# Optimization experiments

Measured on AMD Instinct MI355X. Metric: run time of the kernel, lower is better.

Reference implementation:

```python
import jax, jax.numpy as jnp
import numpy as np

HEAD_SIZE = 64
INPUT_SIZE = 1024
B, T = 8, 2048


def setup_inputs() -> dict:
    key = jax.random.key(0)
    kx, kq, kk, kv = jax.random.split(key, 4)
    x = jax.random.normal(kx, (B, T, INPUT_SIZE), dtype=jnp.float32)
    s = 1.0 / np.sqrt(INPUT_SIZE)
    Wq = jax.random.uniform(kq, (INPUT_SIZE, HEAD_SIZE), minval=-s, maxval=s, dtype=jnp.float32)
    Wk = jax.random.uniform(kk, (INPUT_SIZE, HEAD_SIZE), minval=-s, maxval=s, dtype=jnp.float32)
    Wv = jax.random.uniform(kv, (INPUT_SIZE, HEAD_SIZE), minval=-s, maxval=s, dtype=jnp.float32)
    return {"x": x, "Wq": Wq, "Wk": Wk, "Wv": Wv}


def reference(x, Wq, Wk, Wv):
    # Faithful to the torch module: scores = K @ Q^T (note: keys times queries^T),
    # causal mask on upper triangle of that matrix, softmax over last axis,
    # dropout treated as identity (eval), then scores @ V.
    q = jnp.einsum('bti,ih->bth', x, Wq)  # [B,T,H]
    k = jnp.einsum('bti,ih->bth', x, Wk)
    v = jnp.einsum('bti,ih->bth', x, Wv)
    scale = HEAD_SIZE ** -0.5
    scores = jnp.einsum('bth,bsh->bts', k, q) * scale  # [B,T,T] = K Q^T
    Tlen = x.shape[1]
    causal = jnp.tril(jnp.ones((Tlen, Tlen), dtype=bool))
    scores = jnp.where(causal, scores, -jnp.inf)
    w = jax.nn.softmax(scores, axis=-1)
    out = jnp.einsum('bts,bsh->bth', w, v)  # [B,T,H]
    return out
```

## Files before the change

kernel.cpp:

```cpp
#include <hip/hip_runtime.h>

typedef __bf16 bf16_t;
typedef bf16_t bf16x8 __attribute__((ext_vector_type(8)));
typedef float f32x4 __attribute__((ext_vector_type(4)));

#define NB 8
#define TT 2048
#define DIN 1024
#define HH 64
#define MM (NB * TT)

__device__ __forceinline__ unsigned short f2bf(float f) {
    unsigned int u = __float_as_uint(f);
    u += 0x7fffu + ((u >> 16) & 1u);
    return (unsigned short)(u >> 16);
}

__device__ __forceinline__ int block_detect_f32(const unsigned int* __restrict__ xw,
                                                int tid, int* sflag) {
    if (tid < 64) {
        unsigned int u = xw[tid];
        unsigned int e = (u >> 7) & 0xFFu;
        unsigned long long m = __ballot(e >= 100u && e <= 150u);
        if (tid == 0) *sflag = (__popcll(m) < 48) ? 1 : 0;
    }
    __syncthreads();
    return *sflag;
}

__global__ __launch_bounds__(256) void transpose_w_kernel(
    const void* __restrict__ Wq, const void* __restrict__ Wk,
    const void* __restrict__ Wv, const unsigned int* __restrict__ xw,
    unsigned short* __restrict__ Wt) {
    __shared__ int sflag;
    __shared__ unsigned short ts[64][68];
    const int tid = threadIdx.x;
    const int isf32 = block_detect_f32(xw, tid, &sflag);
    const int w = blockIdx.x >> 4, kt = blockIdx.x & 15;
    const void* W = (w == 0) ? Wq : (w == 1) ? Wk : Wv;
    const int kk = tid >> 4, nn = (tid & 15) * 4;
#pragma unroll
    for (int j = 0; j < 4; ++j) {
        int k = kk + j * 16;
        if (isf32) {
            float4 f = *(const float4*)((const float*)W + (size_t)(kt * 64 + k) * 64 + nn);
            ts[k][nn + 0] = f2bf(f.x); ts[k][nn + 1] = f2bf(f.y);
            ts[k][nn + 2] = f2bf(f.z); ts[k][nn + 3] = f2bf(f.w);
        } else {
            *(uint2*)&ts[k][nn] =
                *(const uint2*)((const unsigned short*)W + (size_t)(kt * 64 + k) * 64 + nn);
        }
    }
    __syncthreads();
    const int n = tid >> 2, k0 = (tid & 3) * 16;
    unsigned short tmp[16];
#pragma unroll
    for (int j = 0; j < 16; ++j) tmp[j] = ts[k0 + j][n];
    unsigned short* dst = Wt + (size_t)(w * 64 + n) * 1024 + kt * 64 + k0;
    *(uint4*)(dst + 0) = *(uint4*)&tmp[0];
    *(uint4*)(dst + 8) = *(uint4*)&tmp[8];
}

__global__ __launch_bounds__(256) void proj_kernel(
    const void* __restrict__ xraw, const unsigned short* __restrict__ Wt,
    unsigned short* __restrict__ qbuf, unsigned short* __restrict__ kbuf,
    unsigned short* __restrict__ vtbuf) {
    __shared__ int sflag;
    __shared__ __align__(16) unsigned short xs[64][72];
    __shared__ __align__(16) unsigned short wts[192][72];

    const int tid = threadIdx.x;
    const int isf32 = block_detect_f32((const unsigned int*)xraw, tid, &sflag);
    const int m0 = blockIdx.x * 64;
    const int wave = tid >> 6, lane = tid & 63, quad = lane >> 4, l15 = lane & 15;
    const int rw = wave & 1, cw = wave >> 1;

    f32x4 acc[2][6];
#pragma unroll
    for (int rt = 0; rt < 2; ++rt)
#pragma unroll
        for (int ct = 0; ct < 6; ++ct)
            acc[rt][ct] = (f32x4){0.f, 0.f, 0.f, 0.f};

    const float* xf = (const float*)xraw;
    const unsigned short* xb = (const unsigned short*)xraw;

    const int xrow = tid >> 2, xkb = (tid & 3) * 16;

    float4 px[4];
    uint4  pxb[2];
    uint4  pw[6];

    auto prefetch = [&](int k0) {
        if (isf32) {
            const float* gp = xf + (size_t)(m0 + xrow) * DIN + k0 + xkb;
#pragma unroll
            for (int j = 0; j < 4; ++j) px[j] = *(const float4*)(gp + j * 4);
        } else {
            const unsigned short* gp = xb + (size_t)(m0 + xrow) * DIN + k0 + xkb;
            pxb[0] = *(const uint4*)(gp + 0);
            pxb[1] = *(const uint4*)(gp + 8);
        }
#pragma unroll
        for (int j = 0; j < 6; ++j) {
            int c = tid + j * 256;
            int row = c >> 3, kc = c & 7;
            pw[j] = *(const uint4*)(Wt + (size_t)row * 1024 + k0 + kc * 8);
        }
    };

    prefetch(0);

    for (int it = 0; it < 16; ++it) {
        __syncthreads();
        if (isf32) {
            unsigned short t[16];
#pragma unroll
            for (int j = 0; j < 4; ++j) {
                t[j * 4 + 0] = f2bf(px[j].x); t[j * 4 + 1] = f2bf(px[j].y);
                t[j * 4 + 2] = f2bf(px[j].z); t[j * 4 + 3] = f2bf(px[j].w);
            }
            *(uint4*)&xs[xrow][xkb + 0] = *(uint4*)&t[0];
            *(uint4*)&xs[xrow][xkb + 8] = *(uint4*)&t[8];
        } else {
            *(uint4*)&xs[xrow][xkb + 0] = pxb[0];
            *(uint4*)&xs[xrow][xkb + 8] = pxb[1];
        }
#pragma unroll
        for (int j = 0; j < 6; ++j) {
            int c = tid + j * 256;
            int row = c >> 3, kc = c & 7;
            *(uint4*)&wts[row][kc * 8] = pw[j];
        }
        __syncthreads();

        if (it < 15) prefetch((it + 1) * 64);

#pragma unroll
        for (int ks = 0; ks < 2; ++ks) {
            bf16x8 a[2], b[6];
#pragma unroll
            for (int rt = 0; rt < 2; ++rt)
                a[rt] = *(const bf16x8*)&xs[rw * 32 + rt * 16 + l15][ks * 32 + quad * 8];
#pragma unroll
            for (int ct = 0; ct < 6; ++ct)
                b[ct] = *(const bf16x8*)&wts[cw * 96 + ct * 16 + l15][ks * 32 + quad * 8];
#pragma unroll
            for (int rt = 0; rt < 2; ++rt)
#pragma unroll
                for (int ct = 0; ct < 6; ++ct)
                    acc[rt][ct] = __builtin_amdgcn_mfma_f32_16x16x32_bf16(
                        a[rt], b[ct], acc[rt][ct], 0, 0, 0);
        }
    }

#pragma unroll
    for (int rt = 0; rt < 2; ++rt)
#pragma unroll
        for (int ct = 0; ct < 6; ++ct) {
            int n = cw * 96 + ct * 16 + l15;
            int wsel = n >> 6, nn = n & 63;
#pragma unroll
            for (int reg = 0; reg < 4; ++reg) {
                int m = m0 + rw * 32 + rt * 16 + quad * 4 + reg;
                unsigned short bv = f2bf(acc[rt][ct][reg]);
                if (wsel == 0)      qbuf[(size_t)m * HH + nn] = bv;
                else if (wsel == 1) kbuf[(size_t)m * HH + nn] = bv;
                else {
                    int bb = m >> 11, t = m & 2047;
                    vtbuf[((size_t)bb * HH + nn) * TT + t] = bv;
                }
            }
        }
}

__global__ __launch_bounds__(256) void attn_kernel(
    const unsigned short* __restrict__ rowbuf,
    const unsigned short* __restrict__ colbuf,
    const unsigned short* __restrict__ vtbuf,
    float* __restrict__ O_part,
    float* __restrict__ l_part) {

    __shared__ __align__(16) unsigned short Qr_s[64][72];
    __shared__ __align__(16) unsigned short Kc_s[64][72];
    __shared__ __align__(16) unsigned short Vt_s[64][72];
    __shared__ __align__(16) unsigned short P_s[4][16][72];

    const int tid  = threadIdx.x;
    const int bx   = blockIdx.x;
    const int b    = blockIdx.y;
    int rt, ch;
    if (bx < 8)       { rt = bx;                 ch = 0; }
    else if (bx < 24) { rt = 8 + ((bx - 8) >> 1);  ch = (bx - 8) & 1; }
    else if (bx < 48) { rt = 16 + (bx - 24) / 3;   ch = (bx - 24) % 3; }
    else              { rt = 24 + ((bx - 48) >> 2); ch = (bx - 48) & 3; }
    const int nct = min(8, rt + 1 - ch * 8);
    const int t0 = rt * 64;
    const int slot = b * 80 + bx;

    const int wave = tid >> 6, lane = tid & 63, quad = lane >> 4, l15 = lane & 15;
    const int sr = tid >> 2, sc = (tid & 3) * 16;

    {
        const uint4* g = (const uint4*)(rowbuf + ((size_t)b * TT + t0 + sr) * HH + sc);
        *(uint4*)&Qr_s[sr][sc + 0] = g[0];
        *(uint4*)&Qr_s[sr][sc + 8] = g[1];
    }

    f32x4 o[4];
#pragma unroll
    for (int c = 0; c < 4; ++c) o[c] = (f32x4){0.f, 0.f, 0.f, 0.f};
    float ls[4] = {0.f, 0.f, 0.f, 0.f};

    const float SCL2 = 0.125f * 1.4426950408889634f;

    for (int i = 0; i < nct; ++i) {
        const int stc = ch * 8 + i;
        const int s0 = stc * 64;
        {
            const uint4* gk = (const uint4*)(colbuf + ((size_t)b * TT + s0 + sr) * HH + sc);
            uint4 k0 = gk[0], k1 = gk[1];
            const uint4* gv = (const uint4*)(vtbuf + ((size_t)b * HH + sr) * TT + s0 + sc);
            uint4 v0 = gv[0], v1 = gv[1];
            *(uint4*)&Kc_s[sr][sc + 0] = k0;
            *(uint4*)&Kc_s[sr][sc + 8] = k1;
            *(uint4*)&Vt_s[sr][sc + 0] = v0;
            *(uint4*)&Vt_s[sr][sc + 8] = v1;
        }
        __syncthreads();

        f32x4 scf[4];
#pragma unroll
        for (int c = 0; c < 4; ++c) scf[c] = (f32x4){0.f, 0.f, 0.f, 0.f};
#pragma unroll
        for (int ks = 0; ks < 2; ++ks) {
            bf16x8 a = *(const bf16x8*)&Qr_s[wave * 16 + l15][ks * 32 + quad * 8];
#pragma unroll
            for (int c = 0; c < 4; ++c) {
                bf16x8 bb = *(const bf16x8*)&Kc_s[c * 16 + l15][ks * 32 + quad * 8];
                scf[c] = __builtin_amdgcn_mfma_f32_16x16x32_bf16(a, bb, scf[c], 0, 0, 0);
            }
        }

        const bool diag = (stc == rt);
#pragma unroll
        for (int r = 0; r < 4; ++r) {
            const int tg = t0 + wave * 16 + quad * 4 + r;
#pragma unroll
            for (int c = 0; c < 4; ++c) {
                float arg = fmaf(scf[c][r], SCL2, -30.f);
                if (diag && (s0 + c * 16 + l15) > tg) arg = -200.f;
                float p = __builtin_amdgcn_exp2f(arg);
                P_s[wave][quad * 4 + r][c * 16 + l15] = f2bf(p);
                ls[r] += p;
            }
        }
#pragma unroll
        for (int ks = 0; ks < 2; ++ks) {
            bf16x8 ap = *(const bf16x8*)&P_s[wave][l15][ks * 32 + quad * 8];
#pragma unroll
            for (int c = 0; c < 4; ++c) {
                bf16x8 bv = *(const bf16x8*)&Vt_s[c * 16 + l15][ks * 32 + quad * 8];
                o[c] = __builtin_amdgcn_mfma_f32_16x16x32_bf16(ap, bv, o[c], 0, 0, 0);
            }
        }
        __syncthreads();
    }

#pragma unroll
    for (int r = 0; r < 4; ++r) {
#pragma unroll
        for (int off = 1; off < 16; off <<= 1) ls[r] += __shfl_xor(ls[r], off);
    }
    if (l15 == 0) {
#pragma unroll
        for (int r = 0; r < 4; ++r)
            l_part[(size_t)slot * 64 + wave * 16 + quad * 4 + r] = ls[r];
    }
#pragma unroll
    for (int c = 0; c < 4; ++c)
#pragma unroll
        for (int r = 0; r < 4; ++r)
            O_part[(size_t)slot * 4096 + (wave * 16 + quad * 4 + r) * 64 + c * 16 + l15] = o[c][r];
}

__global__ __launch_bounds__(256) void combine_kernel(
    const float* __restrict__ O_part, const float* __restrict__ l_part,
    const unsigned int* __restrict__ xw, void* __restrict__ outraw) {
    __shared__ int sflag;
    const int tid = threadIdx.x;
    const int isf32 = block_detect_f32(xw, tid, &sflag);
    const int rt = blockIdx.x, b = blockIdx.y;
    const int nch = rt / 8 + 1;
    const int off = (rt < 8) ? rt : (rt < 16) ? 8 + 2 * (rt - 8)
                   : (rt < 24) ? 24 + 3 * (rt - 16) : 48 + 4 * (rt - 24);
    const int slot0 = b * 80 + off;

    const int row = tid >> 2, cb = (tid & 3) * 16;
    f32x4 a[4];
#pragma unroll
    for (int q = 0; q < 4; ++q) a[q] = (f32x4){0.f, 0.f, 0.f, 0.f};
    float l = 0.f;
    for (int j = 0; j < nch; ++j) {
        const f32x4* p = (const f32x4*)(O_part + (size_t)(slot0 + j) * 4096 + row * 64 + cb);
#pragma unroll
        for (int q = 0; q < 4; ++q) a[q] += p[q];
        l += l_part[(size_t)(slot0 + j) * 64 + row];
    }
    const float inv = 1.f / l;
    const size_t base = ((size_t)b * TT + rt * 64 + row) * HH + cb;
    if (isf32) {
        float* outf = (float*)outraw;
#pragma unroll
        for (int q = 0; q < 4; ++q) {
            f32x4 v = a[q] * inv;
            *(f32x4*)(outf + base + q * 4) = v;
        }
    } else {
        unsigned short h[16];
#pragma unroll
        for (int q = 0; q < 4; ++q)
#pragma unroll
            for (int e = 0; e < 4; ++e) h[q * 4 + e] = f2bf(a[q][e] * inv);
        unsigned short* outb = (unsigned short*)outraw;
        *(uint4*)(outb + base + 0) = *(uint4*)&h[0];
        *(uint4*)(outb + base + 8) = *(uint4*)&h[8];
    }
}

extern "C" void kernel_launch(void* const* d_in, const int* in_sizes, int n_in,
                              void* d_out, int out_size, void* d_ws, size_t ws_size,
                              hipStream_t stream) {
    const void* x  = d_in[0];
    const void* Wq = d_in[1];
    const void* Wk = d_in[2];
    const void* Wv = d_in[3];
    unsigned short* ws = (unsigned short*)d_ws;

    unsigned short* qbuf  = ws;
    unsigned short* kbuf  = ws + (size_t)MM * HH;
    unsigned short* vtbuf = ws + (size_t)2 * MM * HH;
    unsigned short* wtbuf = ws + (size_t)3 * MM * HH;
    float* O_part = (float*)(ws + (size_t)3 * MM * HH + 3 * 65536);
    float* l_part = O_part + (size_t)640 * 4096;

    hipLaunchKernelGGL(transpose_w_kernel, dim3(48), dim3(256), 0, stream,
                       Wq, Wk, Wv, (const unsigned int*)x, wtbuf);
    hipLaunchKernelGGL(proj_kernel, dim3(256), dim3(256), 0, stream,
                       x, wtbuf, qbuf, kbuf, vtbuf);
    hipLaunchKernelGGL(attn_kernel, dim3(80, 8), dim3(256), 0, stream,
                       kbuf, qbuf, vtbuf, O_part, l_part);
    hipLaunchKernelGGL(combine_kernel, dim3(32, 8), dim3(256), 0, stream,
                       O_part, l_part, (const unsigned int*)x, d_out);
}
```

Baseline: 159.6 us.

## Split projection over N, async-load weights to LDS, fuse combine into attention

The projection kernel now splits the 192 output columns across two grid rows (512 blocks instead of 256) and loads the weight tile directly into LDS with global_load_lds, which frees registers and allows two blocks per CU. The separate combine kernel is removed. The last attention block to finish each row tile, detected with an atomic counter that the transpose kernel zeroes, now does the normalisation and writes the output. This removes one launch and adds more parallelism in the projection, at the cost of reading x twice and adding fence and atomic overhead.

New measurement: 278.9 us. +74.8%, slower.

```diff
diff --git a/kernel.cpp b/kernel.cpp
--- a/kernel.cpp
+++ b/kernel.cpp
@@ -14,6 +14,12 @@
     unsigned int u = __float_as_uint(f);
     u += 0x7fffu + ((u >> 16) & 1u);
     return (unsigned short)(u >> 16);
+}
+
+__device__ __forceinline__ void async16(void* l, const void* g) {
+    __builtin_amdgcn_global_load_lds(
+        (const __attribute__((address_space(1))) unsigned int*)g,
+        (__attribute__((address_space(3))) unsigned int*)l, 16, 0, 0);
 }
 
 __device__ __forceinline__ int block_detect_f32(const unsigned int* __restrict__ xw,
@@ -31,10 +37,11 @@
 __global__ __launch_bounds__(256) void transpose_w_kernel(
     const void* __restrict__ Wq, const void* __restrict__ Wk,
     const void* __restrict__ Wv, const unsigned int* __restrict__ xw,
-    unsigned short* __restrict__ Wt) {
+    unsigned short* __restrict__ Wt, int* __restrict__ ctr) {
     __shared__ int sflag;
     __shared__ unsigned short ts[64][68];
     const int tid = threadIdx.x;
+    if (blockIdx.x == 0) ctr[tid] = 0;
     const int isf32 = block_detect_f32(xw, tid, &sflag);
     const int w = blockIdx.x >> 4, kt = blockIdx.x & 15;
     const void* W = (w == 0) ? Wq : (w == 1) ? Wk : Wv;
@@ -61,56 +68,67 @@
     *(uint4*)(dst + 8) = *(uint4*)&tmp[8];
 }
 
-__global__ __launch_bounds__(256) void proj_kernel(
+#define XR 72
+#define WROWC 9
+
+__global__ __launch_bounds__(256, 2) void proj_kernel(
     const void* __restrict__ xraw, const unsigned short* __restrict__ Wt,
     unsigned short* __restrict__ qbuf, unsigned short* __restrict__ kbuf,
     unsigned short* __restrict__ vtbuf) {
     __shared__ int sflag;
-    __shared__ __align__(16) unsigned short xs[64][72];
-    __shared__ __align__(16) unsigned short wts[192][72];
+    __shared__ __align__(16) unsigned short xs[64 * XR];
+    __shared__ __align__(16) unsigned char wlds[96 * WROWC * 16];
 
     const int tid = threadIdx.x;
     const int isf32 = block_detect_f32((const unsigned int*)xraw, tid, &sflag);
     const int m0 = blockIdx.x * 64;
+    const int nh = blockIdx.y;
     const int wave = tid >> 6, lane = tid & 63, quad = lane >> 4, l15 = lane & 15;
     const int rw = wave & 1, cw = wave >> 1;
 
-    f32x4 acc[2][6];
-#pragma unroll
-    for (int rt = 0; rt < 2; ++rt)
-#pragma unroll
-        for (int ct = 0; ct < 6; ++ct)
-            acc[rt][ct] = (f32x4){0.f, 0.f, 0.f, 0.f};
-
     const float* xf = (const float*)xraw;
     const unsigned short* xb = (const unsigned short*)xraw;
-
-    const int xrow = tid >> 2, xkb = (tid & 3) * 16;
-
+    const unsigned char* wg = (const unsigned char*)Wt;
+
+    const unsigned char* wsrc[4];
+    unsigned int wdst[4];
+    int nw = 0;
+#pragma unroll
+    for (int j = 0; j < 4; ++j) {
+        int c = (wave + 4 * j) * 64 + lane;
+        if (c < 864) {
+            int R = c / WROWC, cc = c % WROWC;
+            int ccu = (cc > 7) ? 0 : cc;
+            wsrc[nw] = wg + (size_t)(nh * 96 + R) * 2048 + ccu * 16;
+            wdst[nw] = c * 16;
+            ++nw;
+        }
+    }
+
+    const int xr = tid >> 2, xc = (tid & 3) * 16;
     float4 px[4];
     uint4  pxb[2];
-    uint4  pw[6];
-
-    auto prefetch = [&](int k0) {
+    auto ldx = [&](int k0) {
         if (isf32) {
-            const float* gp = xf + (size_t)(m0 + xrow) * DIN + k0 + xkb;
-#pragma unroll
-            for (int j = 0; j < 4; ++j) px[j] = *(const float4*)(gp + j * 4);
+            const float* g = xf + (size_t)(m0 + xr) * DIN + k0 + xc;
+#pragma unroll
+            for (int j = 0; j < 4; ++j) px[j] = *(const float4*)(g + j * 4);
         } else {
-            const unsigned short* gp = xb + (size_t)(m0 + xrow) * DIN + k0 + xkb;
-            pxb[0] = *(const uint4*)(gp + 0);
-            pxb[1] = *(const uint4*)(gp + 8);
-        }
-#pragma unroll
-        for (int j = 0; j < 6; ++j) {
-            int c = tid + j * 256;
-            int row = c >> 3, kc = c & 7;
-            pw[j] = *(const uint4*)(Wt + (size_t)row * 1024 + k0 + kc * 8);
+            const unsigned short* g = xb + (size_t)(m0 + xr) * DIN + k0 + xc;
+            pxb[0] = *(const uint4*)(g + 0);
+            pxb[1] = *(const uint4*)(g + 8);
         }
     };
 
-    prefetch(0);
-
+    f32x4 acc[2][3];
+#pragma unroll
+    for (int rt = 0; rt < 2; ++rt)
+#pragma unroll
+        for (int ct = 0; ct < 3; ++ct)
+            acc[rt][ct] = (f32x4){0.f, 0.f, 0.f, 0.f};
+
+    ldx(0);
+    size_t woff = 0;
     for (int it = 0; it < 16; ++it) {
         __syncthreads();
         if (isf32) {
@@ -120,35 +138,33 @@
                 t[j * 4 + 0] = f2bf(px[j].x); t[j * 4 + 1] = f2bf(px[j].y);
                 t[j * 4 + 2] = f2bf(px[j].z); t[j * 4 + 3] = f2bf(px[j].w);
             }
-            *(uint4*)&xs[xrow][xkb + 0] = *(uint4*)&t[0];
-            *(uint4*)&xs[xrow][xkb + 8] = *(uint4*)&t[8];
+            *(uint4*)&xs[xr * XR + xc + 0] = *(uint4*)&t[0];
+            *(uint4*)&xs[xr * XR + xc + 8] = *(uint4*)&t[8];
         } else {
-            *(uint4*)&xs[xrow][xkb + 0] = pxb[0];
-            *(uint4*)&xs[xrow][xkb + 8] = pxb[1];
-        }
-#pragma unroll
-        for (int j = 0; j < 6; ++j) {
-            int c = tid + j * 256;
-            int row = c >> 3, kc = c & 7;
-            *(uint4*)&wts[row][kc * 8] = pw[j];
-        }
+            *(uint4*)&xs[xr * XR + xc + 0] = pxb[0];
+            *(uint4*)&xs[xr * XR + xc + 8] = pxb[1];
+        }
+        for (int j = 0; j < nw; ++j) async16(&wlds[wdst[j]], wsrc[j] + woff);
+        woff += 128;
         __syncthreads();
 
-        if (it < 15) prefetch((it + 1) * 64);
+        if (it < 15) ldx((it + 1) * 64);
 
 #pragma unroll
         for (int ks = 0; ks < 2; ++ks) {
-            bf16x8 a[2], b[6];
+            bf16x8 a[2], b[3];
 #pragma unroll
             for (int rt = 0; rt < 2; ++rt)
-                a[rt] = *(const bf16x8*)&xs[rw * 32 + rt * 16 + l15][ks * 32 + quad * 8];
-#pragma unroll
-            for (int ct = 0; ct < 6; ++ct)
-                b[ct] = *(const bf16x8*)&wts[cw * 96 + ct * 16 + l15][ks * 32 + quad * 8];
+                a[rt] = *(const bf16x8*)
+                    &xs[(rw * 32 + rt * 16 + l15) * XR + ks * 32 + quad * 8];
+#pragma unroll
+            for (int ct = 0; ct < 3; ++ct)
+                b[ct] = *(const bf16x8*)
+                    &wlds[(cw * 48 + ct * 16 + l15) * (WROWC * 16) + ks * 64 + quad * 16];
 #pragma unroll
             for (int rt = 0; rt < 2; ++rt)
 #pragma unroll
-                for (int ct = 0; ct < 6; ++ct)
+                for (int ct = 0; ct < 3; ++ct)
                     acc[rt][ct] = __builtin_amdgcn_mfma_f32_16x16x32_bf16(
                         a[rt], b[ct], acc[rt][ct], 0, 0, 0);
         }
@@ -157,8 +173,8 @@
 #pragma unroll
     for (int rt = 0; rt < 2; ++rt)
 #pragma unroll
-        for (int ct = 0; ct < 6; ++ct) {
-            int n = cw * 96 + ct * 16 + l15;
+        for (int ct = 0; ct < 3; ++ct) {
+            int n = nh * 96 + cw * 48 + ct * 16 + l15;
             int wsel = n >> 6, nn = n & 63;
 #pragma unroll
             for (int reg = 0; reg < 4; ++reg) {
@@ -179,14 +195,20 @@
     const unsigned short* __restrict__ colbuf,
     const unsigned short* __restrict__ vtbuf,
     float* __restrict__ O_part,
-    float* __restrict__ l_part) {
-
+    float* __restrict__ l_part,
+    int* __restrict__ ctr,
+    const unsigned int* __restrict__ xw,
+    void* __restrict__ outraw) {
+
+    __shared__ int sflag;
     __shared__ __align__(16) unsigned short Qr_s[64][72];
     __shared__ __align__(16) unsigned short Kc_s[64][72];
     __shared__ __align__(16) unsigned short Vt_s[64][72];
     __shared__ __align__(16) unsigned short P_s[4][16][72];
+    __shared__ int slast;
 
     const int tid  = threadIdx.x;
+    const int isf32 = block_detect_f32(xw, tid, &sflag);
     const int bx   = blockIdx.x;
     const int b    = blockIdx.y;
     int rt, ch;
@@ -282,20 +304,21 @@
 #pragma unroll
         for (int r = 0; r < 4; ++r)
             O_part[(size_t)slot * 4096 + (wave * 16 + quad * 4 + r) * 64 + c * 16 + l15] = o[c][r];
-}
-
-__global__ __launch_bounds__(256) void combine_kernel(
-    const float* __restrict__ O_part, const float* __restrict__ l_part,
-    const unsigned int* __restrict__ xw, void* __restrict__ outraw) {
-    __shared__ int sflag;
-    const int tid = threadIdx.x;
-    const int isf32 = block_detect_f32(xw, tid, &sflag);
-    const int rt = blockIdx.x, b = blockIdx.y;
+
     const int nch = rt / 8 + 1;
+    __threadfence();
+    __syncthreads();
+    if (tid == 0) {
+        int prev = atomicAdd(&ctr[b * 32 + rt], 1);
+        slast = (prev == nch - 1) ? 1 : 0;
+    }
+    __syncthreads();
+    if (!slast) return;
+    __threadfence();
+
     const int off = (rt < 8) ? rt : (rt < 16) ? 8 + 2 * (rt - 8)
                    : (rt < 24) ? 24 + 3 * (rt - 16) : 48 + 4 * (rt - 24);
     const int slot0 = b * 80 + off;
-
     const int row = tid >> 2, cb = (tid & 3) * 16;
     f32x4 a[4];
 #pragma unroll
@@ -343,13 +366,13 @@
     unsigned short* wtbuf = ws + (size_t)3 * MM * HH;
     float* O_part = (float*)(ws + (size_t)3 * MM * HH + 3 * 65536);
     float* l_part = O_part + (size_t)640 * 4096;
+    int*   ctr    = (int*)(l_part + 640 * 64);
 
     hipLaunchKernelGGL(transpose_w_kernel, dim3(48), dim3(256), 0, stream,
-                       Wq, Wk, Wv, (const unsigned int*)x, wtbuf);
-    hipLaunchKernelGGL(proj_kernel, dim3(256), dim3(256), 0, stream,
+                       Wq, Wk, Wv, (const unsigned int*)x, wtbuf, ctr);
+    hipLaunchKernelGGL(proj_kernel, dim3(256, 2), dim3(256), 0, stream,
                        x, wtbuf, qbuf, kbuf, vtbuf);
     hipLaunchKernelGGL(attn_kernel, dim3(80, 8), dim3(256), 0, stream,
-                       kbuf, qbuf, vtbuf, O_part, l_part);
-    hipLaunchKernelGGL(combine_kernel, dim3(32, 8), dim3(256), 0, stream,
-                       O_part, l_part, (const unsigned int*)x, d_out);
-}
+                       kbuf, qbuf, vtbuf, O_part, l_part, ctr,
+                       (const unsigned int*)x, d_out);
+}
```
